# Kernel tuning notes

Measured on AMD Instinct MI355X. Metric: run time of the kernel, lower is better.

## Reference

```python
import jax, jax.numpy as jnp
import numpy as np

GROUP = 64
DIM = 4096
N_HEADS = 32
N_KV = 8
HEAD_DIM = DIM // N_HEADS  # 128
N_REP = N_HEADS // N_KV    # 4
B = 1
S = 2048
THETA = 1e6


def _pack_q40(rng, out_f, in_f):
    """Random int4 weights packed Q4_0 style (two nibbles per int8) + per-group scales."""
    q = rng.integers(-7, 8, size=(out_f * in_f,)).reshape(-1, 2, GROUP)
    packed = ((q[:, 0] << 4) | (q[:, 1] & 15)).astype(np.int8)  # [out*in/group/2, group]
    scale = (np.abs(rng.standard_normal((out_f * in_f // GROUP, 1))) * 0.01 + 1e-3).astype(np.float32)
    return jnp.asarray(packed), jnp.asarray(scale)


def dequantize_q40(w, scale, shape):
    """Faithful port of torch dequantize_q40: arithmetic shifts sign-extend nibbles."""
    msb = jnp.right_shift(w, 4)                          # high nibble, sign-extended
    lsb = jnp.right_shift(jnp.left_shift(w, 4), 4)       # low nibble, sign-extended
    grp = jnp.concatenate([msb, lsb], axis=1).reshape(-1, GROUP)  # hstack then view(-1, group)
    return (grp.astype(scale.dtype) * scale).reshape(shape)


def setup_inputs() -> dict:
    rng = np.random.default_rng(0)
    wq, sq = _pack_q40(rng, N_HEADS * HEAD_DIM, DIM)
    wk, sk = _pack_q40(rng, N_KV * HEAD_DIM, DIM)
    wv, sv = _pack_q40(rng, N_KV * HEAD_DIM, DIM)
    wo, so = _pack_q40(rng, DIM, N_HEADS * HEAD_DIM)
    x = jnp.asarray(rng.standard_normal((B, S, DIM)), jnp.float32)
    inv_freq = 1.0 / (THETA ** (np.arange(0, HEAD_DIM, 2, dtype=np.float64) / HEAD_DIM))
    ang = np.outer(np.arange(S, dtype=np.float64), inv_freq)  # [S, HEAD_DIM/2]
    cos = jnp.asarray(np.cos(ang), jnp.float32)
    sin = jnp.asarray(np.sin(ang), jnp.float32)
    causal = np.triu(np.ones((S, S), dtype=bool), k=1)
    mask = jnp.asarray(np.where(causal, -1e9, 0.0), jnp.float32)
    return dict(x=x, wq=wq, sq=sq, wk=wk, sk=sk, wv=wv, sv=sv, wo=wo, so=so,
                cos=cos, sin=sin, mask=mask)


def _rotate_half(t):
    h = t.shape[-1] // 2
    return jnp.concatenate([-t[..., h:], t[..., :h]], axis=-1)


def reference(x, wq, sq, wk, sk, wv, sv, wo, so, cos, sin, mask):
    # Dequant-then-matmul QKV projections (weights stored as [out, in])
    Wq = dequantize_q40(wq, sq, (N_HEADS * HEAD_DIM, DIM))
    Wk = dequantize_q40(wk, sk, (N_KV * HEAD_DIM, DIM))
    Wv = dequantize_q40(wv, sv, (N_KV * HEAD_DIM, DIM))
    Wo = dequantize_q40(wo, so, (DIM, N_HEADS * HEAD_DIM))

    xq = (x @ Wq.T).reshape(B, S, N_HEADS, HEAD_DIM)
    xk = (x @ Wk.T).reshape(B, S, N_KV, HEAD_DIM)
    xv = (x @ Wv.T).reshape(B, S, N_KV, HEAD_DIM)

    # RoPE (rotate-half convention): cos/sin are [S, HEAD_DIM/2] -> cat to [S, HEAD_DIM]
    cosf = jnp.concatenate([cos, cos], axis=-1)[:, None, :]  # [S, 1, HEAD_DIM]
    sinf = jnp.concatenate([sin, sin], axis=-1)[:, None, :]
    xq = xq * cosf + _rotate_half(xq) * sinf
    xk = xk * cosf + _rotate_half(xk) * sinf

    # start_pos == 0 prefill: keys/values are the freshly projected xk/xv
    # GQA: repeat_interleave over the kv-head dim
    keys = jnp.repeat(xk, N_REP, axis=2)    # [B, S, N_HEADS, HEAD_DIM]
    values = jnp.repeat(xv, N_REP, axis=2)

    scores = jnp.einsum('bqhd,bkhd->bhqk', xq, keys) / np.float32(np.sqrt(HEAD_DIM))
    scores = scores + mask  # additive causal mask broadcast over [B, H]
    attn = jax.nn.softmax(scores, axis=-1)
    out = jnp.einsum('bhqk,bkhd->bqhd', attn, values).reshape(B, S, N_HEADS * HEAD_DIM)
    return out @ Wo.T
```

## Files before the change

### kernel.cpp

```cpp
#include <hip/hip_runtime.h>
#include <stdint.h>

#define DIMX 4096
#define NH   32
#define NKV  8
#define HD   128
#define SEQ  2048
#define QKVD 6144

typedef _Float16 h16;
typedef __attribute__((ext_vector_type(8))) _Float16 h16x8;
typedef __attribute__((ext_vector_type(4))) _Float16 h16x4;
typedef __attribute__((ext_vector_type(4))) float   f32x4;

__device__ __forceinline__ void gload_lds16(const void* g, void* l) {
  __builtin_amdgcn_global_load_lds(
      (const __attribute__((address_space(1))) void*)g,
      (__attribute__((address_space(3))) void*)l, 16, 0, 0);
}

template <int CTRL>
__device__ __forceinline__ float dpp_mv(float x) {
  int y = __builtin_amdgcn_mov_dpp(__builtin_bit_cast(int, x), CTRL, 0xF, 0xF, true);
  return __builtin_bit_cast(float, y);
}
__device__ __forceinline__ float red16_max(float x) {
  x = fmaxf(x, dpp_mv<0xB1>(x));
  x = fmaxf(x, dpp_mv<0x1B>(x));
  x = fmaxf(x, dpp_mv<0x141>(x));
  x = fmaxf(x, dpp_mv<0x140>(x));
  return x;
}
__device__ __forceinline__ float red16_sum(float x) {
  x += dpp_mv<0xB1>(x);
  x += dpp_mv<0x1B>(x);
  x += dpp_mv<0x141>(x);
  x += dpp_mv<0x140>(x);
  return x;
}

__device__ __forceinline__ void dq_unit(const void* __restrict__ w, const float* __restrict__ sc,
                                        h16* __restrict__ out, int u, int flag) {
  uint32_t b4;
  if (flag) {
    const int4 t = *(const int4*)((const int*)w + 4 * u);
    b4 = (uint32_t)(t.x & 0xFF) | ((uint32_t)(t.y & 0xFF) << 8) |
         ((uint32_t)(t.z & 0xFF) << 16) | ((uint32_t)(t.w & 0xFF) << 24);
  } else {
    b4 = ((const uint32_t*)w)[u];
  }
  int r = u >> 4;
  int p = (u & 15) * 4;
  float shi = sc[2 * r], slo = sc[2 * r + 1];
  h16x4 hi, lo;
#pragma unroll
  for (int j = 0; j < 4; ++j) {
    int by = (int)((b4 >> (8 * j)) & 0xFF);
    int hn = (by << 24) >> 28;
    int ln = (by << 28) >> 28;
    hi[j] = (h16)((float)hn * shi);
    lo[j] = (h16)((float)ln * slo);
  }
  *(h16x4*)(out + (r << 7) + p)      = hi;
  *(h16x4*)(out + (r << 7) + 64 + p) = lo;
}

#define U_WQ 2097152
#define U_WK 524288
#define U_WV 524288
#define U_WO 2097152

__global__ __launch_bounds__(256) void prep_all(
    const void* __restrict__ wq, const float* __restrict__ sq,
    const void* __restrict__ wk, const float* __restrict__ sk,
    const void* __restrict__ wv, const float* __restrict__ sv,
    const void* __restrict__ wo, const float* __restrict__ so,
    const float4* __restrict__ x,
    h16* __restrict__ Wqkv, h16* __restrict__ Wo, h16x4* __restrict__ xb) {
  __shared__ int sfl;
  if (threadIdx.x == 0) {
    int ok = 1;
    const int* wi = (const int*)wq;
    for (int i = 0; i < 64; ++i) {
      int v = wi[i];
      if (v < -128 || v > 127) ok = 0;
    }
    sfl = ok;
  }
  __syncthreads();
  const int fl = sfl;
  int u = blockIdx.x * 256 + threadIdx.x;
  if (u < U_WQ) { dq_unit(wq, sq, Wqkv, u, fl); return; }
  u -= U_WQ;
  if (u < U_WK) { dq_unit(wk, sk, Wqkv + 16777216, u, fl); return; }
  u -= U_WK;
  if (u < U_WV) { dq_unit(wv, sv, Wqkv + 20971520, u, fl); return; }
  u -= U_WV;
  if (u < U_WO) { dq_unit(wo, so, Wo, u, fl); return; }
  u -= U_WO;
  {
    float4 v = x[u];
    h16x4 o;
    o.x = (h16)v.x; o.y = (h16)v.y; o.z = (h16)v.z; o.w = (h16)v.w;
    xb[u] = o;
  }
}

template <typename OutT, int NT, int MODE>
__global__ __launch_bounds__(256) void gemm_bt(
    const h16* __restrict__ A, const h16* __restrict__ B,
    OutT* __restrict__ C, int M, int N, int K,
    const float* __restrict__ cosb, const float* __restrict__ sinb,
    h16* __restrict__ vt) {
  constexpr int BN = NT * 32;
  constexpr int SAB = 128 * 64 + BN * 64;
  constexpr int SSZ = (MODE == 1 && 128 * 136 > SAB) ? 128 * 136 : SAB;
  __shared__ __attribute__((aligned(16))) h16 SMEM[SSZ];
  h16* As = SMEM;
  h16* Bs = SMEM + 128 * 64;
  h16* T  = SMEM;

  const int tid  = threadIdx.x;
  const int wv   = tid >> 6, lane = tid & 63;
  const int wr   = wv >> 1,  wc   = wv & 1;
  const int quad = lane >> 4, l15 = lane & 15;
  const int m0 = blockIdx.y * 128, n0 = blockIdx.x * BN;

  f32x4 acc[4][NT];
#pragma unroll
  for (int i = 0; i < 4; ++i)
#pragma unroll
    for (int j = 0; j < NT; ++j) acc[i][j] = (f32x4){0.f, 0.f, 0.f, 0.f};

  const h16* Ab = A + (size_t)m0 * K;
  const h16* Bb = B + (size_t)n0 * K;

  for (int k0 = 0; k0 < K; k0 += 64) {
    __syncthreads();
#pragma unroll
    for (int i = 0; i < 4; ++i) {
      int c = i * 256 + tid;
      int row = c >> 3, cs = c & 7, g = cs ^ (row & 7);
      gload_lds16(Ab + (size_t)row * K + k0 + g * 8, (char*)As + c * 16);
    }
#pragma unroll
    for (int i = 0; i < NT; ++i) {
      int c = i * 256 + tid;
      int row = c >> 3, cs = c & 7, g = cs ^ (row & 7);
      gload_lds16(Bb + (size_t)row * K + k0 + g * 8, (char*)Bs + c * 16);
    }
    __syncthreads();

#pragma unroll
    for (int ks = 0; ks < 2; ++ks) {
      h16x8 af[4], bfr[NT];
#pragma unroll
      for (int mt = 0; mt < 4; ++mt) {
        int row = wr * 64 + mt * 16 + l15;
        af[mt] = *(const h16x8*)&As[row * 64 + (((ks * 4 + quad) ^ (row & 7)) * 8)];
      }
#pragma unroll
      for (int nt = 0; nt < NT; ++nt) {
        int row = wc * (NT * 16) + nt * 16 + l15;
        bfr[nt] = *(const h16x8*)&Bs[row * 64 + (((ks * 4 + quad) ^ (row & 7)) * 8)];
      }
#pragma unroll
      for (int mt = 0; mt < 4; ++mt)
#pragma unroll
        for (int nt = 0; nt < NT; ++nt)
          acc[mt][nt] = __builtin_amdgcn_mfma_f32_16x16x32_f16(af[mt], bfr[nt], acc[mt][nt], 0, 0, 0);
    }
  }

  if (MODE == 1) {
    if (n0 < 5120) {
      __syncthreads();
#pragma unroll
      for (int mt = 0; mt < 4; ++mt)
#pragma unroll
        for (int nt = 0; nt < NT; ++nt)
#pragma unroll
          for (int r = 0; r < 4; ++r)
            T[(wr * 64 + mt * 16 + quad * 4 + r) * 136 + wc * 64 + nt * 16 + l15] =
                (h16)acc[mt][nt][r];
      __syncthreads();
      const int row = tid >> 1, half = tid & 1;
      const size_t gs = (size_t)(m0 + row);
#pragma unroll
      for (int i = 0; i < 8; ++i) {
        int c0 = half * 32 + i * 4;
        h16x4 a = *(const h16x4*)&T[row * 136 + c0];
        h16x4 b = *(const h16x4*)&T[row * 136 + c0 + 64];
        float4 cc = *(const float4*)(cosb + gs * 64 + c0);
        float4 ss = *(const float4*)(sinb + gs * 64 + c0);
        h16x4 oa, ob;
        oa.x = (h16)((float)a.x * cc.x - (float)b.x * ss.x);
        oa.y = (h16)((float)a.y * cc.y - (float)b.y * ss.y);
        oa.z = (h16)((float)a.z * cc.z - (float)b.z * ss.z);
        oa.w = (h16)((float)a.w * cc.w - (float)b.w * ss.w);
        ob.x = (h16)((float)b.x * cc.x + (float)a.x * ss.x);
        ob.y = (h16)((float)b.y * cc.y + (float)a.y * ss.y);
        ob.z = (h16)((float)b.z * cc.z + (float)a.z * ss.z);
        ob.w = (h16)((float)b.w * cc.w + (float)a.w * ss.w);
        *(h16x4*)((h16*)C + gs * N + n0 + c0)      = oa;
        *(h16x4*)((h16*)C + gs * N + n0 + c0 + 64) = ob;
      }
    } else {
      const int kvh = (n0 - 5120) >> 7;
      h16* vbase = vt + (size_t)kvh * HD * SEQ;
#pragma unroll
      for (int mt = 0; mt < 4; ++mt)
#pragma unroll
        for (int nt = 0; nt < NT; ++nt) {
          int d = wc * 64 + nt * 16 + l15;
          int s = m0 + wr * 64 + mt * 16 + quad * 4;
          h16x4 vvv;
#pragma unroll
          for (int r = 0; r < 4; ++r) vvv[r] = (h16)acc[mt][nt][r];
          *(h16x4*)(vbase + (size_t)d * SEQ + s) = vvv;
        }
    }
    return;
  }

#pragma unroll
  for (int mt = 0; mt < 4; ++mt)
#pragma unroll
    for (int nt = 0; nt < NT; ++nt)
#pragma unroll
      for (int r = 0; r < 4; ++r) {
        int row = m0 + wr * 64 + mt * 16 + quad * 4 + r;
        int col = n0 + wc * (NT * 16) + nt * 16 + l15;
        C[(size_t)row * N + col] = (OutT)acc[mt][nt][r];
      }
}

__global__ __launch_bounds__(256, 2) void flash_attn(
    const h16* __restrict__ qkv, const h16* __restrict__ vt, h16* __restrict__ o_out) {
  __shared__ __attribute__((aligned(16))) h16 Ks[64 * 128];
  __shared__ __attribute__((aligned(16))) h16 Vts[128 * 64];
  __shared__ __attribute__((aligned(16))) h16 Ps[4][32 * 72];

  const int tid  = threadIdx.x;
  const int w    = tid >> 6, lane = tid & 63;
  const int quad = lane >> 4, l15 = lane & 15;
  const int h    = blockIdx.x;
  const int y    = blockIdx.y;
  const int qt   = (y < 8) ? (15 - y) : (y - 8);
  const int kv   = h >> 2;
  const int rowq = qt * 128 + w * 32;
  const h16* vtg = vt + (size_t)kv * HD * SEQ;

  h16x8 qf[2][4];
#pragma unroll
  for (int mt = 0; mt < 2; ++mt) {
    const h16* qrow = qkv + (size_t)(rowq + mt * 16 + l15) * QKVD + h * 128;
#pragma unroll
    for (int ks = 0; ks < 4; ++ks)
      qf[mt][ks] = *(const h16x8*)(qrow + ks * 32 + quad * 8);
  }

  f32x4 o[2][8];
#pragma unroll
  for (int mt = 0; mt < 2; ++mt)
#pragma unroll
    for (int i = 0; i < 8; ++i) o[mt][i] = (f32x4){0.f, 0.f, 0.f, 0.f};
  float mrow[2][4], lrow[2][4];
#pragma unroll
  for (int mt = 0; mt < 2; ++mt)
#pragma unroll
    for (int r = 0; r < 4; ++r) { mrow[mt][r] = -3e30f; lrow[mt][r] = 0.f; }
  h16* Psw = Ps[w];

  const int nkt = 2 * qt + 2;
  for (int kt = 0; kt < nkt; ++kt) {
    const int k0 = kt * 64;
    __syncthreads();
#pragma unroll
    for (int i = 0; i < 4; ++i) {
      int c = i * 256 + tid;
      int key = c >> 4, d8s = c & 15;
      gload_lds16(qkv + (size_t)(k0 + key) * QKVD + 4096 + kv * 128 + (d8s ^ (key & 15)) * 8,
                  (char*)Ks + c * 16);
    }
#pragma unroll
    for (int i = 0; i < 4; ++i) {
      int c = i * 256 + tid;
      int d = c >> 3, p = c & 7;
      gload_lds16(vtg + (size_t)d * SEQ + k0 + (p ^ (d & 7)) * 8,
                  (char*)Vts + c * 16);
    }
    __syncthreads();

    if (k0 <= rowq + 31) {
      const float sscale = 0.08838834764831845f;
      float alpha[2][4];
      f32x4 s2[2][4];
#pragma unroll
      for (int nt = 0; nt < 4; ++nt) {
        int key = nt * 16 + l15;
        f32x4 a0 = (f32x4){0.f, 0.f, 0.f, 0.f};
        f32x4 a1 = (f32x4){0.f, 0.f, 0.f, 0.f};
#pragma unroll
        for (int ks = 0; ks < 4; ++ks) {
          int d8 = ks * 4 + quad;
          h16x8 kf = *(const h16x8*)&Ks[key * 128 + ((d8 ^ (key & 15)) * 8)];
          a0 = __builtin_amdgcn_mfma_f32_16x16x32_f16(qf[0][ks], kf, a0, 0, 0, 0);
          a1 = __builtin_amdgcn_mfma_f32_16x16x32_f16(qf[1][ks], kf, a1, 0, 0, 0);
        }
        s2[0][nt] = a0;
        s2[1][nt] = a1;
      }
#pragma unroll
      for (int mt = 0; mt < 2; ++mt) {
#pragma unroll
        for (int r = 0; r < 4; ++r) {
          int rowg = rowq + mt * 16 + quad * 4 + r;
          float pv[4];
          float tm = -3e30f;
#pragma unroll
          for (int nt = 0; nt < 4; ++nt) {
            float v = s2[mt][nt][r] * sscale;
            if (k0 + nt * 16 + l15 > rowg) v = -3e30f;
            pv[nt] = v;
            tm = fmaxf(tm, v);
          }
          tm = red16_max(tm);
          float mnew = fmaxf(mrow[mt][r], tm);
          float a = __expf(mrow[mt][r] - mnew);
          mrow[mt][r] = mnew;
          alpha[mt][r] = a;
          float ps = 0.f;
#pragma unroll
          for (int nt = 0; nt < 4; ++nt) {
            float e = __expf(pv[nt] - mnew);
            ps += e;
            Psw[(mt * 16 + quad * 4 + r) * 72 + nt * 16 + l15] = (h16)e;
          }
          ps = red16_sum(ps);
          lrow[mt][r] = lrow[mt][r] * a + ps;
        }
      }
#pragma unroll
      for (int mt = 0; mt < 2; ++mt)
#pragma unroll
        for (int on = 0; on < 8; ++on) {
          o[mt][on][0] *= alpha[mt][0]; o[mt][on][1] *= alpha[mt][1];
          o[mt][on][2] *= alpha[mt][2]; o[mt][on][3] *= alpha[mt][3];
        }
      asm volatile("s_waitcnt lgkmcnt(0)" ::: "memory");
#pragma unroll
      for (int ks = 0; ks < 2; ++ks) {
        h16x8 pf0 = *(const h16x8*)&Psw[(0  + l15) * 72 + ks * 32 + quad * 8];
        h16x8 pf1 = *(const h16x8*)&Psw[(16 + l15) * 72 + ks * 32 + quad * 8];
        int k8 = ks * 4 + quad;
#pragma unroll
        for (int on = 0; on < 8; ++on) {
          int d = on * 16 + l15;
          h16x8 vf = *(const h16x8*)&Vts[d * 64 + ((k8 ^ (d & 7)) * 8)];
          o[0][on] = __builtin_amdgcn_mfma_f32_16x16x32_f16(pf0, vf, o[0][on], 0, 0, 0);
          o[1][on] = __builtin_amdgcn_mfma_f32_16x16x32_f16(pf1, vf, o[1][on], 0, 0, 0);
        }
      }
    }
  }
#pragma unroll
  for (int mt = 0; mt < 2; ++mt) {
    float linv[4];
#pragma unroll
    for (int r = 0; r < 4; ++r) linv[r] = 1.0f / lrow[mt][r];
#pragma unroll
    for (int on = 0; on < 8; ++on)
#pragma unroll
      for (int r = 0; r < 4; ++r) {
        int row = rowq + mt * 16 + quad * 4 + r;
        int col = h * 128 + on * 16 + l15;
        o_out[(size_t)row * DIMX + col] = (h16)(o[mt][on][r] * linv[r]);
      }
  }
}

extern "C" void kernel_launch(void* const* d_in, const int* in_sizes, int n_in,
                              void* d_out, int out_size, void* d_ws, size_t ws_size,
                              hipStream_t stream) {
  const float* x    = (const float*)d_in[0];
  const void*  wq   = d_in[1];
  const float* sq   = (const float*)d_in[2];
  const void*  wk   = d_in[3];
  const float* sk   = (const float*)d_in[4];
  const void*  wv   = d_in[5];
  const float* sv   = (const float*)d_in[6];
  const void*  wo   = d_in[7];
  const float* so   = (const float*)d_in[8];
  const float* cosb = (const float*)d_in[9];
  const float* sinb = (const float*)d_in[10];
  float* out = (float*)d_out;

  char* ws = (char*)d_ws;
  h16* Wqkv = (h16*)ws;
  h16* Wo   = (h16*)(ws + 50331648);
  h16* xb   = (h16*)(ws + 83886080);
  h16* qkv  = (h16*)(ws + 100663296);
  h16* vt   = (h16*)d_out;

  prep_all<<<28672, 256, 0, stream>>>(wq, sq, wk, sk, wv, sv, wo, so,
                                      (const float4*)x, Wqkv, Wo, (h16x4*)xb);

  gemm_bt<h16, 4, 1><<<dim3(48, 16), 256, 0, stream>>>(
      xb, Wqkv, qkv, SEQ, QKVD, DIMX, cosb, sinb, vt);

  flash_attn<<<dim3(32, 16), 256, 0, stream>>>(qkv, vt, xb);

  gemm_bt<float, 2, 0><<<dim3(64, 16), 256, 0, stream>>>(
      xb, Wo, out, SEQ, DIMX, DIMX, cosb, sinb, vt);
}
```

Measured before the change: 490.3 us.

## Add 256x256 pipelined QKV GEMM kernel and widen output GEMM tile

Adds a new 512-thread QKV projection kernel that computes 256x256 output tiles. It uses a swizzled double-buffered LDS pipeline built on direct global-to-LDS loads, split into four sub-tile phases with explicit waitcnt and barrier scheduling. RoPE is applied through an LDS transpose stage in the epilogue, and the V columns are written transposed. The output projection GEMM also switches to a wider N tile (NT=4) on a 32x16 grid. The goal is higher MFMA utilisation and less global traffic per FLOP, at the cost of heavy LDS use (128KB) and fewer, larger blocks (192 for QKV), which may leave some CUs idle.

```diff
diff --git a/kernel.cpp b/kernel.cpp
--- a/kernel.cpp
+++ b/kernel.cpp
@@ -235,6 +235,179 @@
       }
 }
 
+__global__ __launch_bounds__(512, 2) void gemm256_qkv(
+    const h16* __restrict__ A, const h16* __restrict__ B, h16* __restrict__ C,
+    int M, int N, int K,
+    const float* __restrict__ cosb, const float* __restrict__ sinb,
+    h16* __restrict__ vt) {
+  __shared__ __attribute__((aligned(16))) h16 SM[65536];
+  h16* T = SM;
+
+  const int tid  = threadIdx.x;
+  const int w    = tid >> 6, lane = tid & 63;
+  const int wr   = w >> 2, wc = w & 3;
+  const int quad = lane >> 4, l15 = lane & 15;
+  const int axr  = l15 & 7;
+  const int m0 = blockIdx.y * 256, n0 = blockIdx.x * 256;
+
+  const h16* Ab = A + (size_t)m0 * K;
+  const h16* Bb = B + (size_t)n0 * K;
+  const int srow = tid >> 3;
+  const int sg8  = ((tid & 7) ^ (srow & 7)) * 8;
+
+  f32x4 acc[2][2][4][2];
+#pragma unroll
+  for (int a = 0; a < 2; ++a)
+#pragma unroll
+    for (int b = 0; b < 2; ++b)
+#pragma unroll
+      for (int mt = 0; mt < 4; ++mt)
+#pragma unroll
+        for (int nt = 0; nt < 2; ++nt) acc[a][b][mt][nt] = (f32x4){0.f, 0.f, 0.f, 0.f};
+
+  h16x8 af[4][2], bf[2][2];
+
+#define STG(sl_, tile_) do {                                                        \
+    const h16* g_ = ((sl_) == 0) ? Ab : ((sl_) == 1) ? (Bb + (size_t)128 * K)       \
+                  : ((sl_) == 2) ? (Ab + (size_t)128 * K) : Bb;                     \
+    char* d_ = (char*)(SM + (((tile_) & 1) ? 32768 : 0) + (sl_) * 8192);            \
+    const int kk_ = (tile_) * 64;                                                   \
+    gload_lds16(g_ + (size_t)srow * K + kk_ + sg8, d_ + tid * 16);                  \
+    gload_lds16(g_ + (size_t)(srow + 64) * K + kk_ + sg8, d_ + (512 + tid) * 16);   \
+  } while (0)
+
+#define LDA_(tile_, a_) do {                                                        \
+    const h16* s_ = SM + (((tile_) & 1) ? 32768 : 0) + ((a_) ? 2 : 0) * 8192;       \
+    _Pragma("unroll") for (int mt = 0; mt < 4; ++mt)                                \
+    _Pragma("unroll") for (int ks = 0; ks < 2; ++ks)                                \
+      af[mt][ks] = *(const h16x8*)&s_[(wr * 64 + mt * 16 + l15) * 64 +              \
+                                      (((ks * 4 + quad) ^ axr) * 8)];               \
+  } while (0)
+
+#define LDB_(tile_, b_) do {                                                        \
+    const h16* s_ = SM + (((tile_) & 1) ? 32768 : 0) + ((b_) ? 1 : 3) * 8192;       \
+    _Pragma("unroll") for (int nt = 0; nt < 2; ++nt)                                \
+    _Pragma("unroll") for (int ks = 0; ks < 2; ++ks)                                \
+      bf[nt][ks] = *(const h16x8*)&s_[(wc * 32 + nt * 16 + l15) * 64 +              \
+                                      (((ks * 4 + quad) ^ axr) * 8)];               \
+  } while (0)
+
+#define MMA_(a_, b_) do {                                                           \
+    __builtin_amdgcn_s_setprio(1);                                                  \
+    _Pragma("unroll") for (int mt = 0; mt < 4; ++mt)                                \
+    _Pragma("unroll") for (int nt = 0; nt < 2; ++nt)                                \
+    _Pragma("unroll") for (int ks = 0; ks < 2; ++ks)                                \
+      acc[a_][b_][mt][nt] = __builtin_amdgcn_mfma_f32_16x16x32_f16(                 \
+          af[mt][ks], bf[nt][ks], acc[a_][b_][mt][nt], 0, 0, 0);                    \
+    __builtin_amdgcn_s_setprio(0);                                                  \
+  } while (0)
+
+#define CFENCE asm volatile("" ::: "memory")
+#define BARX do { CFENCE; __builtin_amdgcn_s_barrier(); CFENCE; } while (0)
+#define LG0 do { asm volatile("s_waitcnt lgkmcnt(0)" ::: "memory");                 \
+                 __builtin_amdgcn_sched_barrier(0); } while (0)
+#define VM6 asm volatile("s_waitcnt vmcnt(6)" ::: "memory")
+#define VM0 asm volatile("s_waitcnt vmcnt(0)" ::: "memory")
+
+  const int NTILE = K >> 6;
+  const int NIT   = NTILE >> 1;
+
+  STG(0, 0); STG(1, 0); STG(2, 0); STG(3, 0);
+  STG(0, 1); STG(1, 1); STG(2, 1);
+  VM6;
+  BARX;
+
+  for (int t = 0; t < NIT; ++t) {
+    const int t0 = 2 * t, t1 = 2 * t + 1;
+    const int t2 = (2 * t + 2 < NTILE) ? 2 * t + 2 : NTILE - 1;
+    const int t3 = (2 * t + 3 < NTILE) ? 2 * t + 3 : NTILE - 1;
+    LDA_(t0, 0); LDB_(t0, 0); STG(3, t1);
+    BARX; LG0; MMA_(0, 0); BARX;
+    LDB_(t0, 1); STG(0, t2);
+    BARX; LG0; MMA_(0, 1); BARX;
+    LDA_(t0, 1); STG(1, t2);
+    BARX; LG0; MMA_(1, 1); BARX;
+    LDB_(t0, 0); STG(2, t2);
+    BARX; LG0; MMA_(1, 0); VM6; BARX;
+    LDA_(t1, 0); LDB_(t1, 0); STG(3, t2);
+    BARX; LG0; MMA_(0, 0); BARX;
+    LDB_(t1, 1); STG(0, t3);
+    BARX; LG0; MMA_(0, 1); BARX;
+    LDA_(t1, 1); STG(1, t3);
+    BARX; LG0; MMA_(1, 1); BARX;
+    LDB_(t1, 0); STG(2, t3);
+    BARX; LG0; MMA_(1, 0); VM6; BARX;
+  }
+
+  VM0;
+  BARX;
+
+  if (n0 < 5120) {
+#pragma unroll
+    for (int hh = 0; hh < 2; ++hh) {
+      if (hh) __syncthreads();
+#pragma unroll
+      for (int a = 0; a < 2; ++a)
+#pragma unroll
+        for (int mt = 0; mt < 4; ++mt)
+#pragma unroll
+          for (int nt = 0; nt < 2; ++nt)
+#pragma unroll
+            for (int r = 0; r < 4; ++r)
+              T[(a * 128 + wr * 64 + mt * 16 + quad * 4 + r) * 136 +
+                wc * 32 + nt * 16 + l15] = (h16)acc[a][hh][mt][nt][r];
+      __syncthreads();
+      const int row = tid >> 1, half = tid & 1;
+      const size_t gs = (size_t)(m0 + row);
+#pragma unroll
+      for (int i = 0; i < 8; ++i) {
+        int c0 = half * 32 + i * 4;
+        h16x4 a4 = *(const h16x4*)&T[row * 136 + c0];
+        h16x4 b4 = *(const h16x4*)&T[row * 136 + c0 + 64];
+        float4 cc = *(const float4*)(cosb + gs * 64 + c0);
+        float4 ss = *(const float4*)(sinb + gs * 64 + c0);
+        h16x4 oa, ob;
+        oa.x = (h16)((float)a4.x * cc.x - (float)b4.x * ss.x);
+        oa.y = (h16)((float)a4.y * cc.y - (float)b4.y * ss.y);
+        oa.z = (h16)((float)a4.z * cc.z - (float)b4.z * ss.z);
+        oa.w = (h16)((float)a4.w * cc.w - (float)b4.w * ss.w);
+        ob.x = (h16)((float)b4.x * cc.x + (float)a4.x * ss.x);
+        ob.y = (h16)((float)b4.y * cc.y + (float)a4.y * ss.y);
+        ob.z = (h16)((float)b4.z * cc.z + (float)a4.z * ss.z);
+        ob.w = (h16)((float)b4.w * cc.w + (float)a4.w * ss.w);
+        *(h16x4*)(C + gs * N + n0 + hh * 128 + c0)      = oa;
+        *(h16x4*)(C + gs * N + n0 + hh * 128 + c0 + 64) = ob;
+      }
+    }
+  } else {
+    const int kvb = (n0 - 5120) >> 7;
+#pragma unroll
+    for (int a = 0; a < 2; ++a)
+#pragma unroll
+      for (int b = 0; b < 2; ++b)
+#pragma unroll
+        for (int mt = 0; mt < 4; ++mt)
+#pragma unroll
+          for (int nt = 0; nt < 2; ++nt) {
+            int d = wc * 32 + nt * 16 + l15;
+            int s = m0 + a * 128 + wr * 64 + mt * 16 + quad * 4;
+            h16x4 vvv;
+#pragma unroll
+            for (int r = 0; r < 4; ++r) vvv[r] = (h16)acc[a][b][mt][nt][r];
+            *(h16x4*)(vt + (size_t)(kvb + b) * HD * SEQ + (size_t)d * SEQ + s) = vvv;
+          }
+  }
+#undef STG
+#undef LDA_
+#undef LDB_
+#undef MMA_
+#undef CFENCE
+#undef BARX
+#undef LG0
+#undef VM6
+#undef VM0
+}
+
 __global__ __launch_bounds__(256, 2) void flash_attn(
     const h16* __restrict__ qkv, const h16* __restrict__ vt, h16* __restrict__ o_out) {
   __shared__ __attribute__((aligned(16))) h16 Ks[64 * 128];
@@ -406,11 +579,11 @@
   prep_all<<<28672, 256, 0, stream>>>(wq, sq, wk, sk, wv, sv, wo, so,
                                       (const float4*)x, Wqkv, Wo, (h16x4*)xb);
 
-  gemm_bt<h16, 4, 1><<<dim3(48, 16), 256, 0, stream>>>(
+  gemm256_qkv<<<dim3(24, 8), 512, 0, stream>>>(
       xb, Wqkv, qkv, SEQ, QKVD, DIMX, cosb, sinb, vt);
 
   flash_attn<<<dim3(32, 16), 256, 0, stream>>>(qkv, vt, xb);
 
-  gemm_bt<float, 2, 0><<<dim3(64, 16), 256, 0, stream>>>(
+  gemm_bt<float, 4, 0><<<dim3(32, 16), 256, 0, stream>>>(
       xb, Wo, out, SEQ, DIMX, DIMX, cosb, sinb, vt);
 }
```

Result: faster. 465.4 us (-5.1%).

## Replace QKV GEMM with 256x192 pipelined kernel and interleave RoPE weight rows

Applied to the files above, without the earlier changes.

Adds a dedicated 512-thread QKV GEMM with 256x192 tiles, double-buffered direct-to-LDS loads and hand-placed waitcnt/barrier scheduling with MFMA priority boosts. Q/K weight rows are permuted at dequant time so rotate-half pairs land in adjacent columns, letting RoPE be applied in registers via a DPP lane swap instead of an LDS transpose. The output projection GEMM also switches to a wider N tile. Intended to raise MFMA utilization and operand reuse in the dominant GEMMs. The hand-tuned sync scheme and row permutation are fragile, and the RoPE epilogue now does scattered scalar cos/sin loads and 2-byte stores.

```diff
diff --git a/kernel.cpp b/kernel.cpp
--- a/kernel.cpp
+++ b/kernel.cpp
@@ -39,6 +39,7 @@
   return x;
 }
 
+template <int PERM>
 __device__ __forceinline__ void dq_unit(const void* __restrict__ w, const float* __restrict__ sc,
                                         h16* __restrict__ out, int u, int flag) {
   uint32_t b4;
@@ -61,8 +62,16 @@
     hi[j] = (h16)((float)hn * shi);
     lo[j] = (h16)((float)ln * slo);
   }
-  *(h16x4*)(out + (r << 7) + p)      = hi;
-  *(h16x4*)(out + (r << 7) + 64 + p) = lo;
+  size_t base;
+  if (PERM) {
+    int row  = r >> 5;
+    int rowp = (row & ~127) | (((row & 63) << 1) | ((row >> 6) & 1));
+    base = ((size_t)rowp << 12) + (size_t)((r & 31) << 7);
+  } else {
+    base = (size_t)r << 7;
+  }
+  *(h16x4*)(out + base + p)      = hi;
+  *(h16x4*)(out + base + 64 + p) = lo;
 }
 
 #define U_WQ 2097152
@@ -90,13 +99,13 @@
   __syncthreads();
   const int fl = sfl;
   int u = blockIdx.x * 256 + threadIdx.x;
-  if (u < U_WQ) { dq_unit(wq, sq, Wqkv, u, fl); return; }
+  if (u < U_WQ) { dq_unit<1>(wq, sq, Wqkv, u, fl); return; }
   u -= U_WQ;
-  if (u < U_WK) { dq_unit(wk, sk, Wqkv + 16777216, u, fl); return; }
+  if (u < U_WK) { dq_unit<1>(wk, sk, Wqkv + 16777216, u, fl); return; }
   u -= U_WK;
-  if (u < U_WV) { dq_unit(wv, sv, Wqkv + 20971520, u, fl); return; }
+  if (u < U_WV) { dq_unit<0>(wv, sv, Wqkv + 20971520, u, fl); return; }
   u -= U_WV;
-  if (u < U_WO) { dq_unit(wo, so, Wo, u, fl); return; }
+  if (u < U_WO) { dq_unit<0>(wo, so, Wo, u, fl); return; }
   u -= U_WO;
   {
     float4 v = x[u];
@@ -113,12 +122,10 @@
     const float* __restrict__ cosb, const float* __restrict__ sinb,
     h16* __restrict__ vt) {
   constexpr int BN = NT * 32;
-  constexpr int SAB = 128 * 64 + BN * 64;
-  constexpr int SSZ = (MODE == 1 && 128 * 136 > SAB) ? 128 * 136 : SAB;
+  constexpr int SSZ = 128 * 64 + BN * 64;
   __shared__ __attribute__((aligned(16))) h16 SMEM[SSZ];
   h16* As = SMEM;
   h16* Bs = SMEM + 128 * 64;
-  h16* T  = SMEM;
 
   const int tid  = threadIdx.x;
   const int wv   = tid >> 6, lane = tid & 63;
@@ -172,57 +179,6 @@
     }
   }
 
-  if (MODE == 1) {
-    if (n0 < 5120) {
-      __syncthreads();
-#pragma unroll
-      for (int mt = 0; mt < 4; ++mt)
-#pragma unroll
-        for (int nt = 0; nt < NT; ++nt)
-#pragma unroll
-          for (int r = 0; r < 4; ++r)
-            T[(wr * 64 + mt * 16 + quad * 4 + r) * 136 + wc * 64 + nt * 16 + l15] =
-                (h16)acc[mt][nt][r];
-      __syncthreads();
-      const int row = tid >> 1, half = tid & 1;
-      const size_t gs = (size_t)(m0 + row);
-#pragma unroll
-      for (int i = 0; i < 8; ++i) {
-        int c0 = half * 32 + i * 4;
-        h16x4 a = *(const h16x4*)&T[row * 136 + c0];
-        h16x4 b = *(const h16x4*)&T[row * 136 + c0 + 64];
-        float4 cc = *(const float4*)(cosb + gs * 64 + c0);
-        float4 ss = *(const float4*)(sinb + gs * 64 + c0);
-        h16x4 oa, ob;
-        oa.x = (h16)((float)a.x * cc.x - (float)b.x * ss.x);
-        oa.y = (h16)((float)a.y * cc.y - (float)b.y * ss.y);
-        oa.z = (h16)((float)a.z * cc.z - (float)b.z * ss.z);
-        oa.w = (h16)((float)a.w * cc.w - (float)b.w * ss.w);
-        ob.x = (h16)((float)b.x * cc.x + (float)a.x * ss.x);
-        ob.y = (h16)((float)b.y * cc.y + (float)a.y * ss.y);
-        ob.z = (h16)((float)b.z * cc.z + (float)a.z * ss.z);
-        ob.w = (h16)((float)b.w * cc.w + (float)a.w * ss.w);
-        *(h16x4*)((h16*)C + gs * N + n0 + c0)      = oa;
-        *(h16x4*)((h16*)C + gs * N + n0 + c0 + 64) = ob;
-      }
-    } else {
-      const int kvh = (n0 - 5120) >> 7;
-      h16* vbase = vt + (size_t)kvh * HD * SEQ;
-#pragma unroll
-      for (int mt = 0; mt < 4; ++mt)
-#pragma unroll
-        for (int nt = 0; nt < NT; ++nt) {
-          int d = wc * 64 + nt * 16 + l15;
-          int s = m0 + wr * 64 + mt * 16 + quad * 4;
-          h16x4 vvv;
-#pragma unroll
-          for (int r = 0; r < 4; ++r) vvv[r] = (h16)acc[mt][nt][r];
-          *(h16x4*)(vbase + (size_t)d * SEQ + s) = vvv;
-        }
-    }
-    return;
-  }
-
 #pragma unroll
   for (int mt = 0; mt < 4; ++mt)
 #pragma unroll
@@ -233,6 +189,147 @@
         int col = n0 + wc * (NT * 16) + nt * 16 + l15;
         C[(size_t)row * N + col] = (OutT)acc[mt][nt][r];
       }
+}
+
+__global__ __launch_bounds__(512, 2) void gemm192_qkv(
+    const h16* __restrict__ A, const h16* __restrict__ B, h16* __restrict__ C,
+    const float* __restrict__ cosb, const float* __restrict__ sinb,
+    h16* __restrict__ vt) {
+  constexpr int K = DIMX;
+  __shared__ __attribute__((aligned(16))) h16 SM[57344];
+
+  const int tid  = threadIdx.x;
+  const int w    = tid >> 6, lane = tid & 63;
+  const int wr   = w >> 1, wc = w & 1;
+  const int quad = lane >> 4, l15 = lane & 15;
+  const int m0 = blockIdx.y * 256, n0 = blockIdx.x * 192;
+
+  const h16* Ab = A + (size_t)m0 * K;
+  const h16* Bb = B + (size_t)n0 * K;
+  const int srow = tid >> 3;
+  const int sg8  = ((tid & 7) ^ (srow & 7)) * 8;
+
+  f32x4 acc[2][2][2][3];
+#pragma unroll
+  for (int a = 0; a < 2; ++a)
+#pragma unroll
+    for (int b = 0; b < 2; ++b)
+#pragma unroll
+      for (int mt = 0; mt < 2; ++mt)
+#pragma unroll
+        for (int nt = 0; nt < 3; ++nt) acc[a][b][mt][nt] = (f32x4){0.f, 0.f, 0.f, 0.f};
+
+  h16x8 af[2][2];
+  h16x8 bf[2][3][2];
+
+#define STG(sl_, tile_) do {                                                        \
+    const h16* g_ = ((sl_) < 4) ? (Ab + (size_t)((sl_) * 64) * K)                   \
+                                : (Bb + (size_t)(((sl_) - 4) * 64) * K);            \
+    char* d_ = (char*)(SM + ((tile_) & 1) * 28672 + (sl_) * 4096);                  \
+    gload_lds16(g_ + (size_t)srow * K + (tile_) * 64 + sg8, d_ + tid * 16);         \
+  } while (0)
+
+#define LDA_(tile_, a_) do {                                                        \
+    const h16* s_ = SM + ((tile_) & 1) * 28672 + wr * 4096;                         \
+    _Pragma("unroll") for (int mt = 0; mt < 2; ++mt)                                \
+    _Pragma("unroll") for (int ks = 0; ks < 2; ++ks) {                              \
+      int row_ = (a_) * 32 + mt * 16 + l15;                                         \
+      af[mt][ks] = *(const h16x8*)&s_[row_ * 64 + (((ks * 4 + quad) ^ (row_ & 7)) * 8)]; \
+    }                                                                               \
+  } while (0)
+
+#define LDB_(tile_, b_) do {                                                        \
+    const h16* s_ = SM + ((tile_) & 1) * 28672 + 16384;                             \
+    _Pragma("unroll") for (int nt = 0; nt < 3; ++nt)                                \
+    _Pragma("unroll") for (int ks = 0; ks < 2; ++ks) {                              \
+      int row_ = (b_) * 96 + wc * 48 + nt * 16 + l15;                               \
+      bf[b_][nt][ks] = *(const h16x8*)&s_[row_ * 64 + (((ks * 4 + quad) ^ (row_ & 7)) * 8)]; \
+    }                                                                               \
+  } while (0)
+
+#define MMA_(a_, b_) do {                                                           \
+    __builtin_amdgcn_s_setprio(1);                                                  \
+    _Pragma("unroll") for (int mt = 0; mt < 2; ++mt)                                \
+    _Pragma("unroll") for (int nt = 0; nt < 3; ++nt)                                \
+    _Pragma("unroll") for (int ks = 0; ks < 2; ++ks)                                \
+      acc[a_][b_][mt][nt] = __builtin_amdgcn_mfma_f32_16x16x32_f16(                 \
+          af[mt][ks], bf[b_][nt][ks], acc[a_][b_][mt][nt], 0, 0, 0);                \
+    __builtin_amdgcn_s_setprio(0);                                                  \
+  } while (0)
+
+#define CFENCE asm volatile("" ::: "memory")
+#define BARX do { CFENCE; __builtin_amdgcn_s_barrier(); CFENCE; } while (0)
+#define LG0  asm volatile("s_waitcnt lgkmcnt(0)" ::: "memory")
+#define LKH8 asm volatile("s_waitcnt lgkmcnt(8)" ::: "memory")
+#define VM5  asm volatile("s_waitcnt vmcnt(5)" ::: "memory")
+#define VM0  asm volatile("s_waitcnt vmcnt(0)" ::: "memory")
+
+  const int NT2 = K >> 6;
+
+  STG(4, 0); STG(5, 0); STG(6, 0); STG(0, 0); STG(1, 0);
+  STG(2, 0); STG(3, 0);
+  STG(4, 1); STG(5, 1); STG(6, 1); STG(0, 1); STG(1, 1);
+  VM5;
+  BARX;
+
+  for (int t = 0; t < NT2; ++t) {
+    const int tp1 = (t + 1 < NT2) ? t + 1 : NT2 - 1;
+    const int tp2 = (t + 2 < NT2) ? t + 2 : NT2 - 1;
+    LDA_(t, 0); LDB_(t, 0);
+    STG(2, tp1); STG(3, tp1);
+    LKH8;
+    BARX; LG0; MMA_(0, 0); BARX;
+    LDB_(t, 1);
+    STG(4, tp2);
+    BARX; LG0; MMA_(0, 1); BARX;
+    LDA_(t, 1);
+    STG(5, tp2);
+    BARX; LG0; MMA_(1, 1); BARX;
+    STG(6, tp2); STG(0, tp2); STG(1, tp2);
+    BARX; MMA_(1, 0); VM5; BARX;
+  }
+  VM0;
+
+#pragma unroll
+  for (int a = 0; a < 2; ++a)
+#pragma unroll
+    for (int b = 0; b < 2; ++b)
+#pragma unroll
+      for (int mt = 0; mt < 2; ++mt)
+#pragma unroll
+        for (int nt = 0; nt < 3; ++nt) {
+          const int cb   = n0 + b * 96 + wc * 48 + nt * 16;
+          const int row0 = m0 + wr * 64 + a * 32 + mt * 16 + quad * 4;
+          if (cb >= 5120) {
+            const int dcol = cb + l15 - 5120;
+            h16x4 vvv;
+#pragma unroll
+            for (int r = 0; r < 4; ++r) vvv[r] = (h16)acc[a][b][mt][nt][r];
+            *(h16x4*)(vt + (size_t)dcol * SEQ + row0) = vvv;
+          } else {
+            const int col = cb + l15;
+            const int j   = (col & 127) >> 1;
+            const float sgn = (col & 1) ? 1.f : -1.f;
+#pragma unroll
+            for (int r = 0; r < 4; ++r) {
+              float own = acc[a][b][mt][nt][r];
+              float par = dpp_mv<0xB1>(own);
+              float cc  = cosb[(size_t)(row0 + r) * 64 + j];
+              float ss  = sinb[(size_t)(row0 + r) * 64 + j];
+              C[(size_t)(row0 + r) * QKVD + col] = (h16)(own * cc + sgn * par * ss);
+            }
+          }
+        }
+#undef STG
+#undef LDA_
+#undef LDB_
+#undef MMA_
+#undef CFENCE
+#undef BARX
+#undef LG0
+#undef LKH8
+#undef VM5
+#undef VM0
 }
 
 __global__ __launch_bounds__(256, 2) void flash_attn(
@@ -406,11 +503,10 @@
   prep_all<<<28672, 256, 0, stream>>>(wq, sq, wk, sk, wv, sv, wo, so,
                                       (const float4*)x, Wqkv, Wo, (h16x4*)xb);
 
-  gemm_bt<h16, 4, 1><<<dim3(48, 16), 256, 0, stream>>>(
-      xb, Wqkv, qkv, SEQ, QKVD, DIMX, cosb, sinb, vt);
+  gemm192_qkv<<<dim3(32, 8), 512, 0, stream>>>(xb, Wqkv, qkv, cosb, sinb, vt);
 
   flash_attn<<<dim3(32, 16), 256, 0, stream>>>(qkv, vt, xb);
 
-  gemm_bt<float, 2, 0><<<dim3(64, 16), 256, 0, stream>>>(
+  gemm_bt<float, 4, 0><<<dim3(32, 16), 256, 0, stream>>>(
       xb, Wo, out, SEQ, DIMX, DIMX, cosb, sinb, vt);
 }
```

Result: faster. 457.8 us (-6.6%).
